# Kernel optimization log

Measured on AMD Instinct MI355X. Metric: run time of the kernel, lower is better.

## Reference

```python
import jax, jax.numpy as jnp
import numpy as np

V = 100000   # nodes
E = 1600000  # edges (avg degree 16)
LN = 64      # feat_dim
S = 8        # stat_dim
T = 4        # recurrence steps
MU = 0.9
N_EDGE_TYPES = 10


def _uniform_linear(kw, kb, fan_out, fan_in):
    # torch nn.Linear default init: U(-1/sqrt(fan_in), 1/sqrt(fan_in))
    lim = 1.0 / np.sqrt(fan_in)
    W = jax.random.uniform(kw, (fan_out, fan_in), jnp.float32, -lim, lim)
    b = jax.random.uniform(kb, (fan_out,), jnp.float32, -lim, lim)
    return W, b


def setup_inputs() -> dict:
    key = jax.random.key(0)
    ks = jax.random.split(key, 12)
    feat_Matrix = jax.random.normal(ks[0], (V, LN), jnp.float32)
    X_Node = jax.random.randint(ks[1], (E,), 1, V + 1, dtype=jnp.int64)   # 1-indexed
    X_Neis = jax.random.randint(ks[2], (E,), 1, V + 1, dtype=jnp.int64)   # 1-indexed
    edge_type_index = jax.random.randint(ks[3], (E,), 1, N_EDGE_TYPES + 1, dtype=jnp.int32)
    dg_list = jax.random.randint(ks[4], (E,), 1, 65).astype(jnp.float32)  # degrees >= 1
    H_init = jax.random.uniform(ks[5], (V, S), jnp.float32)  # torch.rand init of state
    W_xi, b_xi = _uniform_linear(ks[6], ks[7], S * S, 2 * LN + N_EDGE_TYPES)
    W_rou, b_rou = _uniform_linear(ks[8], ks[9], S, LN)
    W1, b1 = _uniform_linear(ks[10], ks[11], 1, S)
    return {
        "feat_Matrix": feat_Matrix, "X_Node": X_Node, "X_Neis": X_Neis,
        "edge_type_index": edge_type_index, "dg_list": dg_list, "H_init": H_init,
        "W_xi": W_xi, "b_xi": b_xi, "W_rou": W_rou, "b_rou": b_rou,
        "W1": W1, "b1": b1,
    }


def reference(feat_Matrix, X_Node, X_Neis, edge_type_index, dg_list, H_init,
              W_xi, b_xi, W_rou, b_rou, W1, b1):
    src = X_Node - 1           # 0-indexed source nodes
    dst = X_Neis - 1           # 0-indexed neighbor nodes (for embedding gather)
    node_emb = feat_Matrix[src]            # [E, LN]
    neis_emb = feat_Matrix[dst]            # [E, LN]
    et = jax.nn.one_hot(edge_type_index - 1, N_EDGE_TYPES, dtype=jnp.float32)
    X = jnp.concatenate([node_emb, neis_emb, et], axis=1)  # [E, 2*LN+10]

    # Xi(X): per-edge transition matrices A, constant across steps -> precompute
    A = jnp.tanh(X @ W_xi.T + b_xi).reshape(-1, S, S)
    A = A * (MU / S) / dg_list[:, None, None]              # [E, S, S]
    # Rou(neis_emb): per-edge bias b, constant across steps
    bias = jnp.tanh(neis_emb @ W_rou.T + b_rou)            # [E, S]

    def step(H, _):
        He = H[src]                                        # gather [E, S]
        out = jnp.einsum('eij,ej->ei', A, He) + bias       # per-edge small matmul
        # AggrSum: dense one-hot mask vs RAW 1-indexed X_Neis against range(0,V-1)
        # -> scatter by 1-indexed ids; ids == V fall out of range and are dropped.
        Hn = jax.ops.segment_sum(out, X_Neis, num_segments=V)
        return Hn, None

    H, _ = jax.lax.scan(step, H_init, None, length=T)      # [V, S]

    logits = (H @ W1.T + b1).squeeze(-1)                   # [V]
    attn = jax.nn.softmax(logits)                          # softmax over nodes
    graph_out = jnp.tanh(jnp.sum(H * attn[:, None], axis=0))  # [S]
    return graph_out
```

## Files before the change

kernel.cpp:

```cpp
#include <hip/hip_runtime.h>
#include <hip/hip_bf16.h>

constexpr int V   = 100000;
constexpr int E   = 1600000;
constexpr int NET = 10;
constexpr int KXW = 138;
constexpr int NB  = (V + 255) / 256;
constexpr int GN  = 8;
constexpr int NEB = E / 256;
constexpr float MUS   = 0.1125f;
constexpr float SP    = 0.025f;
constexpr float LOG2E = 1.44269504f;
constexpr float S2L   = 2.0f * SP * LOG2E;
constexpr float K7    = MUS / 7.0f;

typedef __attribute__((ext_vector_type(8))) short short8;
typedef __attribute__((ext_vector_type(4))) float float4v;

__device__ __forceinline__ float fast_tanh(float x) {
    return 1.0f - 2.0f * __builtin_amdgcn_rcpf(__expf(2.0f * x) + 1.0f);
}
__device__ __forceinline__ float bflo(unsigned u) { return __uint_as_float(u << 16); }
__device__ __forceinline__ float bfhi(unsigned u) { return __uint_as_float(u & 0xffff0000u); }
__device__ __forceinline__ short f2bf(float x) {
    union { __hip_bfloat16 b; short s; } u; u.b = __float2bfloat16(x); return u.s;
}

__device__ __forceinline__ float ub0(unsigned u) {
#if __has_builtin(__builtin_amdgcn_cvt_f32_ubyte0)
    return __builtin_amdgcn_cvt_f32_ubyte0(u);
#else
    return (float)(u & 0xff);
#endif
}
__device__ __forceinline__ float ub1(unsigned u) {
#if __has_builtin(__builtin_amdgcn_cvt_f32_ubyte1)
    return __builtin_amdgcn_cvt_f32_ubyte1(u);
#else
    return (float)((u >> 8) & 0xff);
#endif
}
__device__ __forceinline__ float ub2(unsigned u) {
#if __has_builtin(__builtin_amdgcn_cvt_f32_ubyte2)
    return __builtin_amdgcn_cvt_f32_ubyte2(u);
#else
    return (float)((u >> 16) & 0xff);
#endif
}
__device__ __forceinline__ float ub3(unsigned u) {
#if __has_builtin(__builtin_amdgcn_cvt_f32_ubyte3)
    return __builtin_amdgcn_cvt_f32_ubyte3(u);
#else
    return (float)(u >> 24);
#endif
}

__device__ __forceinline__ int dot8i4(unsigned a, unsigned b, int c) {
#if __has_builtin(__builtin_amdgcn_sdot8)
    return __builtin_amdgcn_sdot8((int)a, (int)b, c, false);
#else
    int r = c;
    #pragma unroll
    for (int j = 0; j < 8; ++j) {
        int av = ((int)(a << (28 - 4 * j))) >> 28;
        int bv = ((int)(b << (28 - 4 * j))) >> 28;
        r += av * bv;
    }
    return r;
#endif
}

__global__ __launch_bounds__(256) void histg_kernel(
    const int* __restrict__ xneis, int* __restrict__ countg,
    int* __restrict__ rank0)
{
    int e = blockIdx.x * 256 + threadIdx.x;
    if (e >= E) return;
    int g = blockIdx.x & (GN - 1);
    int nr = xneis[e];
    if (nr < V) rank0[e] = atomicAdd(&countg[g * V + nr], 1);
}

__global__ __launch_bounds__(256) void scanV_kernel(
    const int* __restrict__ countg, int* __restrict__ offg,
    int* __restrict__ cnt_tot, int* __restrict__ scanned, int* __restrict__ bsum)
{
    __shared__ int s[256];
    int tid = threadIdx.x;
    int i = blockIdx.x * 256 + tid;
    int c = 0;
    if (i < V) {
        int run = 0;
        #pragma unroll
        for (int g = 0; g < GN; ++g) {
            offg[g * V + i] = run;
            run += countg[g * V + i];
        }
        cnt_tot[i] = run;
        c = run;
    }
    s[tid] = c; __syncthreads();
    #pragma unroll
    for (int off = 1; off < 256; off <<= 1) {
        int t = (tid >= off) ? s[tid - off] : 0;
        __syncthreads();
        s[tid] += t;
        __syncthreads();
    }
    if (i < V) scanned[i] = s[tid] - c;
    if (tid == 255) bsum[blockIdx.x] = s[255];
}

__global__ __launch_bounds__(512) void scan_tops_kernel(
    const int* __restrict__ blocksum, int* __restrict__ tops, int* __restrict__ rowptr)
{
    __shared__ int s[512];
    int tid = threadIdx.x;
    int v = (tid < NB) ? blocksum[tid] : 0;
    s[tid] = v; __syncthreads();
    #pragma unroll
    for (int off = 1; off < 512; off <<= 1) {
        int t = (tid >= off) ? s[tid - off] : 0;
        __syncthreads();
        s[tid] += t;
        __syncthreads();
    }
    if (tid < NB) tops[tid] = s[tid] - v;
    if (tid == 511) rowptr[V] = s[511];
}

__global__ __launch_bounds__(256) void add_offsets_kernel(
    const int* __restrict__ scanned, const int* __restrict__ tops, int* __restrict__ rowptr)
{
    int i = blockIdx.x * 256 + threadIdx.x;
    if (i < V) rowptr[i] = scanned[i] + tops[blockIdx.x];
}

__global__ __launch_bounds__(256) void scatterA_kernel(
    const int* __restrict__ xnode, const int* __restrict__ xneis,
    const int* __restrict__ etype, const float* __restrict__ dg,
    const int* __restrict__ rowptr, const int* __restrict__ offg,
    const int* __restrict__ rank0, uint2* __restrict__ buc,
    int* __restrict__ bcnt)
{
    __shared__ int wcnt[4][8];
    __shared__ int woff[4][8];
    int tid = threadIdx.x;
    int lane = tid & 63, wv = tid >> 6;
    int e = blockIdx.x * 256 + tid;
    int g = blockIdx.x & (GN - 1);

    int nr = xneis[e];
    bool keep = (nr < V);
    int p = -1, r = 0;
    if (keep) {
        p = rowptr[nr] + offg[g * V + nr] + rank0[e];
        r = p >> 18;
    }

    unsigned rnk = 0;
    #pragma unroll
    for (int r8 = 0; r8 < 8; ++r8) {
        unsigned long long m = __ballot(keep && (r == r8));
        if (keep && r == r8)
            rnk = (unsigned)__popcll(m & ((1ull << lane) - 1ull));
        if (lane == 0) wcnt[wv][r8] = (int)__popcll(m);
    }
    __syncthreads();
    if (tid < 8) {
        int run = 0;
        #pragma unroll
        for (int w = 0; w < 4; ++w) { woff[w][tid] = run; run += wcnt[w][tid]; }
        bcnt[blockIdx.x * 8 + tid] = run;
    }
    __syncthreads();

    if (keep) {
        unsigned src = (unsigned)(xnode[e] - 1);
        unsigned et  = (unsigned)(etype[e] - 1);
        unsigned dgi = (unsigned)dg[e] - 1;
        unsigned meta = src | (et << 17) | (dgi << 21);
        int slot = blockIdx.x * 2048 + r * 256 + woff[wv][r] + (int)rnk;
        buc[slot] = make_uint2((unsigned)p, meta);
    }
}

__global__ __launch_bounds__(256) void drain_kernel(
    const uint2* __restrict__ buc, const int* __restrict__ bcnt,
    unsigned* __restrict__ pmeta)
{
    int r = blockIdx.x & 7;
    int nstride = (int)(gridDim.x >> 3);
    for (int sb = (int)(blockIdx.x >> 3); sb < NEB; sb += nstride) {
        int c = bcnt[sb * 8 + r];
        const uint2* seg = buc + (size_t)sb * 2048 + r * 256;
        for (int i = threadIdx.x; i < c; i += 256) {
            uint2 t = seg[i];
            pmeta[t.x] = t.y;
        }
    }
}

__global__ __launch_bounds__(256) void bsum_kernel(
    const float* __restrict__ feat, const int* __restrict__ count,
    const float* __restrict__ Wrou, const float* __restrict__ brou,
    const float* __restrict__ Hinit, float* __restrict__ Bsum,
    uint2* __restrict__ Hq0)
{
    __shared__ float Wl[512];
    __shared__ float bl[8];
    int tid = threadIdx.x;
    for (int i = tid; i < 512; i += 256) Wl[i] = Wrou[i];
    if (tid < 8) bl[tid] = brou[tid];
    __syncthreads();

    int v = blockIdx.x * 256 + tid;
    if (v >= V) return;
    int c = count[v];
    float out[8] = {0, 0, 0, 0, 0, 0, 0, 0};
    if (c > 0) {
        const float4* f4 = (const float4*)(feat + (size_t)(v - 1) * 64);
        float acc[8];
        #pragma unroll
        for (int s = 0; s < 8; ++s) acc[s] = bl[s];
        #pragma unroll 4
        for (int k = 0; k < 16; ++k) {
            float4 x = f4[k];
            #pragma unroll
            for (int s = 0; s < 8; ++s) {
                const float* w = &Wl[s * 64 + k * 4];
                acc[s] += x.x * w[0] + x.y * w[1] + x.z * w[2] + x.w * w[3];
            }
        }
        float fc = (float)c;
        #pragma unroll
        for (int s = 0; s < 8; ++s) out[s] = fc * fast_tanh(acc[s]);
    }
    float4* O = (float4*)(Bsum + (size_t)v * 8);
    O[0] = make_float4(out[0], out[1], out[2], out[3]);
    O[1] = make_float4(out[4], out[5], out[6], out[7]);

    const float4* Hh4 = (const float4*)(Hinit + (size_t)v * 8);
    float4 h0 = Hh4[0], h1 = Hh4[1];
    float hv[8] = {h0.x, h0.y, h0.z, h0.w, h1.x, h1.y, h1.z, h1.w};
    float mx = 0.0f;
    #pragma unroll
    for (int i = 0; i < 8; ++i) mx = fmaxf(mx, fabsf(hv[i]));
    float si = (mx > 0.0f) ? 7.0f / mx : 0.0f;
    unsigned w = 0;
    #pragma unroll
    for (int i = 0; i < 8; ++i)
        w |= ((unsigned)((int)rintf(hv[i] * si)) & 0xFu) << (4 * i);
    Hq0[v] = make_uint2(w, __float_as_uint(mx * (1.0f / 7.0f)));
}

__global__ __launch_bounds__(256) void pq_kernel(
    const float* __restrict__ feat, const float* __restrict__ Wxi,
    unsigned char* __restrict__ P8, ushort* __restrict__ Qb)
{
    const int lane = threadIdx.x & 63, wave = threadIdx.x >> 6;
    const int quad = lane >> 4, l16 = lane & 15;

    short8 bP[4][2], bQ[4][2];
    #pragma unroll
    for (int nt = 0; nt < 4; ++nt) {
        #pragma unroll
        for (int ks = 0; ks < 2; ++ks) {
            const float* wp = Wxi + (size_t)(nt * 16 + l16) * KXW + ks * 32 + quad * 8;
            short8 p, q;
            #pragma unroll
            for (int j = 0; j < 8; ++j) { p[j] = f2bf(wp[j]); q[j] = f2bf(wp[64 + j]); }
            bP[nt][ks] = p; bQ[nt][ks] = q;
        }
    }

    int t = blockIdx.x * 4 + wave;
    if (t >= V / 16) return;
    int v0 = t * 16;

    const float* fp = feat + (size_t)(v0 + l16) * 64 + quad * 8;
    short8 a0, a1;
    #pragma unroll
    for (int j = 0; j < 8; ++j) { a0[j] = f2bf(fp[j]); a1[j] = f2bf(fp[32 + j]); }

    float4v accP[4], accQ[4];
    #pragma unroll
    for (int nt = 0; nt < 4; ++nt) {
        float4v z = {0.f, 0.f, 0.f, 0.f};
        z = __builtin_amdgcn_mfma_f32_16x16x32_bf16(a0, bP[nt][0], z, 0, 0, 0);
        z = __builtin_amdgcn_mfma_f32_16x16x32_bf16(a1, bP[nt][1], z, 0, 0, 0);
        accP[nt] = z;
        float4v w = {0.f, 0.f, 0.f, 0.f};
        w = __builtin_amdgcn_mfma_f32_16x16x32_bf16(a0, bQ[nt][0], w, 0, 0, 0);
        w = __builtin_amdgcn_mfma_f32_16x16x32_bf16(a1, bQ[nt][1], w, 0, 0, 0);
        accQ[nt] = w;
    }

    #pragma unroll
    for (int r = 0; r < 4; ++r) {
        int row = v0 + quad * 4 + r;
        #pragma unroll
        for (int nt = 0; nt < 4; ++nt) {
            int col = nt * 16 + l16;
            int q8 = (int)rintf(accP[nt][r] * (1.0f / SP)) + 128;
            q8 = min(max(q8, 0), 255);
            P8[row * 64 + col] = (unsigned char)q8;
            Qb[row * 64 + col] = (ushort)f2bf(accQ[nt][r]);
        }
    }
}

__global__ __launch_bounds__(256) void amat_kernel(
    const unsigned* __restrict__ pmeta, const int* __restrict__ rowptr,
    const unsigned char* __restrict__ P8, const ushort* __restrict__ Qb,
    const float* __restrict__ Wxi, const float* __restrict__ bxi,
    const uint2* __restrict__ Hq0, const float* __restrict__ Bsum,
    unsigned* __restrict__ A4, uint2* __restrict__ HqOut)
{
    __shared__ float Wet2[NET * 64];
    int tid = threadIdx.x;
    for (int i = tid; i < NET * 64; i += 256) {
        int et = i >> 6, n = i & 63;
        Wet2[i] = 2.0f * LOG2E * (Wxi[n * KXW + 128 + et] + bxi[n]);
    }
    __syncthreads();

    int v = blockIdx.x * 4 + (tid >> 6);
    if (v >= V) return;
    int lane = tid & 63;
    int el = lane >> 3, s = lane & 7;

    const int off = rowptr[v];
    const int deg = rowptr[v + 1] - off;

    float q0, q1, q2, q3, q4, q5, q6, q7;
    {
        uint4 qu = *(const uint4*)(Qb + v * 64 + s * 8);
        const float B = 128.0f * SP, C = 2.0f * LOG2E;
        q0 = C * (bflo(qu.x) - B); q1 = C * (bfhi(qu.x) - B);
        q2 = C * (bflo(qu.y) - B); q3 = C * (bfhi(qu.y) - B);
        q4 = C * (bflo(qu.z) - B); q5 = C * (bfhi(qu.z) - B);
        q6 = C * (bflo(qu.w) - B); q7 = C * (bfhi(qu.w) - B);
    }

    float accD = 0.0f;

    for (int base = 0; base < deg; base += 64) {
        unsigned m_mine = 0;
        {
            int i1 = base + lane;
            if (i1 < deg) m_mine = pmeta[off + i1];
        }
        int nb = deg - base;
        for (int k = 0; k * 8 + el < nb && k < 8; ++k) {
            int ib = k * 8 + el;
            int i = base + ib;
            unsigned m = __shfl(m_mine, ib);
            int src = (int)(m & 0x1FFFF);
            int et  = (int)((m >> 17) & 0xF);

            uint2 pu = *(const uint2*)(P8 + src * 64 + s * 8);
            const float4* w4 = (const float4*)(&Wet2[et * 64 + s * 8]);
            float4 wa = w4[0], wb = w4[1];
            uint2 hq = Hq0[src];

            float r0 = __builtin_amdgcn_rcpf(__builtin_amdgcn_exp2f(fmaf(ub0(pu.x), S2L, q0 + wa.x)) + 1.0f);
            float r1 = __builtin_amdgcn_rcpf(__builtin_amdgcn_exp2f(fmaf(ub1(pu.x), S2L, q1 + wa.y)) + 1.0f);
            float r2 = __builtin_amdgcn_rcpf(__builtin_amdgcn_exp2f(fmaf(ub2(pu.x), S2L, q2 + wa.z)) + 1.0f);
            float r3 = __builtin_amdgcn_rcpf(__builtin_amdgcn_exp2f(fmaf(ub3(pu.x), S2L, q3 + wa.w)) + 1.0f);
            float r4 = __builtin_amdgcn_rcpf(__builtin_amdgcn_exp2f(fmaf(ub0(pu.y), S2L, q4 + wb.x)) + 1.0f);
            float r5 = __builtin_amdgcn_rcpf(__builtin_amdgcn_exp2f(fmaf(ub1(pu.y), S2L, q5 + wb.y)) + 1.0f);
            float r6 = __builtin_amdgcn_rcpf(__builtin_amdgcn_exp2f(fmaf(ub2(pu.y), S2L, q6 + wb.z)) + 1.0f);
            float r7 = __builtin_amdgcn_rcpf(__builtin_amdgcn_exp2f(fmaf(ub3(pu.y), S2L, q7 + wb.w)) + 1.0f);

            int n0 = (int)rintf(fmaf(r0, -14.0f, 7.0f));
            int n1 = (int)rintf(fmaf(r1, -14.0f, 7.0f));
            int n2 = (int)rintf(fmaf(r2, -14.0f, 7.0f));
            int n3 = (int)rintf(fmaf(r3, -14.0f, 7.0f));
            int n4 = (int)rintf(fmaf(r4, -14.0f, 7.0f));
            int n5 = (int)rintf(fmaf(r5, -14.0f, 7.0f));
            int n6 = (int)rintf(fmaf(r6, -14.0f, 7.0f));
            int n7 = (int)rintf(fmaf(r7, -14.0f, 7.0f));

            unsigned w = ((unsigned)n0 & 0xFu)        | (((unsigned)n1 & 0xFu) << 4)
                       | (((unsigned)n2 & 0xFu) << 8)  | (((unsigned)n3 & 0xFu) << 12)
                       | (((unsigned)n4 & 0xFu) << 16) | (((unsigned)n5 & 0xFu) << 20)
                       | (((unsigned)n6 & 0xFu) << 24) | (((unsigned)n7 & 0xFu) << 28);
            A4[(unsigned)(off + i) * 8u + (unsigned)s] = w;

            int dd = dot8i4(w, hq.x, 0);
            float rdg = __builtin_amdgcn_rcpf((float)((int)(m >> 21) + 1));
            accD = fmaf((float)dd, __uint_as_float(hq.y) * rdg, accD);
        }
    }
    accD += __shfl_xor(accD, 8);  accD += __shfl_xor(accD, 16); accD += __shfl_xor(accD, 32);
    float h1v = accD * K7 + Bsum[v * 8 + s];

    float mx = fabsf(h1v);
    mx = fmaxf(mx, __shfl_xor(mx, 1));
    mx = fmaxf(mx, __shfl_xor(mx, 2));
    mx = fmaxf(mx, __shfl_xor(mx, 4));
    float si = (mx > 0.0f) ? 7.0f / mx : 0.0f;
    unsigned nib = (unsigned)((int)rintf(h1v * si)) & 0xFu;
    unsigned b1 = __shfl(nib, lane + 1), b2 = __shfl(nib, lane + 2), b3 = __shfl(nib, lane + 3);
    unsigned b4 = __shfl(nib, lane + 4), b5 = __shfl(nib, lane + 5);
    unsigned b6 = __shfl(nib, lane + 6), b7 = __shfl(nib, lane + 7);
    if (lane == 0) {
        unsigned w = nib | (b1 << 4) | (b2 << 8) | (b3 << 12)
                   | (b4 << 16) | (b5 << 20) | (b6 << 24) | (b7 << 28);
        HqOut[v] = make_uint2(w, __float_as_uint(mx * (1.0f / 7.0f)));
    }
}

__global__ __launch_bounds__(256) void step_kernel(
    const uint2* __restrict__ HqIn, uint2* __restrict__ HqOut,
    const unsigned* __restrict__ pmeta, const int* __restrict__ rowptr,
    const unsigned* __restrict__ A4, const float* __restrict__ Bsum,
    const float* __restrict__ W1, const float* __restrict__ b1,
    float* __restrict__ logitsOut, float* __restrict__ HfpOut)
{
    int v = blockIdx.x * 64 + (threadIdx.x >> 2);
    if (v >= V) return;
    int q = threadIdx.x & 3;

    int p0 = rowptr[v], p1 = rowptr[v + 1];

    float accE0 = 0.0f, accO0 = 0.0f, accE1 = 0.0f, accO1 = 0.0f;
    int p = p0;
    for (; p + 1 < p1; p += 2) {
        unsigned m0 = pmeta[p], m1 = pmeta[p + 1];
        uint2 au0 = *(const uint2*)(A4 + (unsigned)p * 8u + (unsigned)(q * 2));
        uint2 au1 = *(const uint2*)(A4 + (unsigned)(p + 1) * 8u + (unsigned)(q * 2));
        uint2 hq0 = HqIn[m0 & 0x1FFFFu];
        uint2 hq1 = HqIn[m1 & 0x1FFFFu];

        int dE0 = dot8i4(au0.x, hq0.x, 0);
        int dO0 = dot8i4(au0.y, hq0.x, 0);
        float rdg0 = __builtin_amdgcn_rcpf((float)((int)(m0 >> 21) + 1));
        float sc0 = __uint_as_float(hq0.y) * rdg0;
        accE0 = fmaf((float)dE0, sc0, accE0);
        accO0 = fmaf((float)dO0, sc0, accO0);

        int dE1 = dot8i4(au1.x, hq1.x, 0);
        int dO1 = dot8i4(au1.y, hq1.x, 0);
        float rdg1 = __builtin_amdgcn_rcpf((float)((int)(m1 >> 21) + 1));
        float sc1 = __uint_as_float(hq1.y) * rdg1;
        accE1 = fmaf((float)dE1, sc1, accE1);
        accO1 = fmaf((float)dO1, sc1, accO1);
    }
    if (p < p1) {
        unsigned m = pmeta[p];
        uint2 au = *(const uint2*)(A4 + (unsigned)p * 8u + (unsigned)(q * 2));
        uint2 hq = HqIn[m & 0x1FFFFu];
        int dE = dot8i4(au.x, hq.x, 0);
        int dO = dot8i4(au.y, hq.x, 0);
        float rdg = __builtin_amdgcn_rcpf((float)((int)(m >> 21) + 1));
        float sc = __uint_as_float(hq.y) * rdg;
        accE0 = fmaf((float)dE, sc, accE0);
        accO0 = fmaf((float)dO, sc, accO0);
    }
    float accE = accE0 + accE1;
    float accO = accO0 + accO1;

    float hE = accE * K7 + Bsum[v * 8 + q * 2];
    float hO = accO * K7 + Bsum[v * 8 + q * 2 + 1];

    float mx = fmaxf(fabsf(hE), fabsf(hO));
    mx = fmaxf(mx, __shfl_xor(mx, 1));
    mx = fmaxf(mx, __shfl_xor(mx, 2));
    float si = (mx > 0.0f) ? 7.0f / mx : 0.0f;
    unsigned nE = (unsigned)((int)rintf(hE * si)) & 0xFu;
    unsigned nO = (unsigned)((int)rintf(hO * si)) & 0xFu;
    unsigned wq = (nE | (nO << 4)) << (8 * q);
    wq |= __shfl_xor(wq, 1);
    wq |= __shfl_xor(wq, 2);
    if (q == 0)
        HqOut[v] = make_uint2(wq, __float_as_uint(mx * (1.0f / 7.0f)));
    if (HfpOut != nullptr)
        *(float2*)(HfpOut + v * 8 + q * 2) = make_float2(hE, hO);
    if (logitsOut != nullptr) {
        float t = hE * W1[q * 2] + hO * W1[q * 2 + 1];
        t += __shfl_xor(t, 1); t += __shfl_xor(t, 2);
        if (q == 0) logitsOut[v] = t + b1[0];
    }
}

__global__ __launch_bounds__(256) void sum_kernel(
    const float* __restrict__ H, const float* __restrict__ logits,
    float* __restrict__ partial)
{
    float m = -INFINITY, se = 0.0f;
    float sh[8] = {0, 0, 0, 0, 0, 0, 0, 0};
    for (int v = blockIdx.x * 256 + threadIdx.x; v < V; v += 64 * 256) {
        float l = logits[v];
        float mn = fmaxf(m, l);
        float a = __expf(m - mn);
        float w = __expf(l - mn);
        se = se * a + w;
        const float4* H4 = (const float4*)(H + (size_t)v * 8);
        float4 h0 = H4[0], h1 = H4[1];
        sh[0] = sh[0] * a + w * h0.x; sh[1] = sh[1] * a + w * h0.y;
        sh[2] = sh[2] * a + w * h0.z; sh[3] = sh[3] * a + w * h0.w;
        sh[4] = sh[4] * a + w * h1.x; sh[5] = sh[5] * a + w * h1.y;
        sh[6] = sh[6] * a + w * h1.z; sh[7] = sh[7] * a + w * h1.w;
        m = mn;
    }
    #pragma unroll
    for (int o = 1; o < 64; o <<= 1) {
        float mo = __shfl_xor(m, o), seo = __shfl_xor(se, o);
        float sho[8];
        #pragma unroll
        for (int i = 0; i < 8; ++i) sho[i] = __shfl_xor(sh[i], o);
        float mn = fmaxf(m, mo);
        float a = __expf(m - mn), b = __expf(mo - mn);
        se = se * a + seo * b;
        #pragma unroll
        for (int i = 0; i < 8; ++i) sh[i] = sh[i] * a + sho[i] * b;
        m = mn;
    }
    __shared__ float sm[4][10];
    int wv = threadIdx.x >> 6;
    if ((threadIdx.x & 63) == 0) {
        sm[wv][0] = m; sm[wv][9] = se;
        #pragma unroll
        for (int i = 0; i < 8; ++i) sm[wv][1 + i] = sh[i];
    }
    __syncthreads();
    if (threadIdx.x == 0) {
        float M = sm[0][0], SE = 0.0f, SH[8] = {0, 0, 0, 0, 0, 0, 0, 0};
        #pragma unroll
        for (int w2 = 1; w2 < 4; ++w2) M = fmaxf(M, sm[w2][0]);
        #pragma unroll
        for (int w2 = 0; w2 < 4; ++w2) {
            float a = __expf(sm[w2][0] - M);
            SE += sm[w2][9] * a;
            #pragma unroll
            for (int i = 0; i < 8; ++i) SH[i] += sm[w2][1 + i] * a;
        }
        partial[blockIdx.x * 12 + 0] = M;
        partial[blockIdx.x * 12 + 9] = SE;
        #pragma unroll
        for (int i = 0; i < 8; ++i) partial[blockIdx.x * 12 + 1 + i] = SH[i];
    }
}

__global__ void final_kernel(const float* __restrict__ partial, float* __restrict__ out)
{
    int lane = threadIdx.x;
    float m = partial[lane * 12 + 0];
    float se = partial[lane * 12 + 9];
    float sh[8];
    #pragma unroll
    for (int i = 0; i < 8; ++i) sh[i] = partial[lane * 12 + 1 + i];
    #pragma unroll
    for (int o = 1; o < 64; o <<= 1) {
        float mo = __shfl_xor(m, o), seo = __shfl_xor(se, o);
        float sho[8];
        #pragma unroll
        for (int i = 0; i < 8; ++i) sho[i] = __shfl_xor(sh[i], o);
        float mn = fmaxf(m, mo);
        float a = __expf(m - mn), b = __expf(mo - mn);
        se = se * a + seo * b;
        #pragma unroll
        for (int i = 0; i < 8; ++i) sh[i] = sh[i] * a + sho[i] * b;
        m = mn;
    }
    if (lane < 8) out[lane] = tanhf(sh[lane] / se);
}

extern "C" void kernel_launch(void* const* d_in, const int* in_sizes, int n_in,
                              void* d_out, int out_size, void* d_ws, size_t ws_size,
                              hipStream_t stream)
{
    const float* feat  = (const float*)d_in[0];
    const int*   xnode = (const int*)d_in[1];
    const int*   xneis = (const int*)d_in[2];
    const int*   etype = (const int*)d_in[3];
    const float* dg    = (const float*)d_in[4];
    const float* Hinit = (const float*)d_in[5];
    const float* Wxi   = (const float*)d_in[6];
    const float* bxi   = (const float*)d_in[7];
    const float* Wrou  = (const float*)d_in[8];
    const float* brou  = (const float*)d_in[9];
    const float* W1    = (const float*)d_in[10];
    const float* b1    = (const float*)d_in[11];

    char* ws = (char*)d_ws;
    auto alloc = [&](size_t bytes) -> char* {
        char* p = ws; ws += (bytes + 255) & ~(size_t)255; return p;
    };
    unsigned* A4      = (unsigned*)alloc((size_t)E * 32);
    uint2*    buc     = (uint2*)alloc((size_t)NEB * 2048 * 8);
    unsigned char* P8 = (unsigned char*)alloc((size_t)V * 64);
    ushort*   Qb      = (ushort*)alloc((size_t)V * 64 * 2);
    unsigned* pmeta   = (unsigned*)alloc((size_t)E * 4);
    int*      rank0   = (int*)alloc((size_t)E * 4);
    int*      countg  = (int*)alloc((size_t)GN * V * 4);
    int*      offg    = (int*)alloc((size_t)GN * V * 4);
    int*      bcnt    = (int*)alloc((size_t)NEB * 8 * 4);
    int*      cnt     = (int*)alloc((size_t)V * 4);
    int*      scanned = (int*)alloc((size_t)V * 4);
    int*      rowptr  = (int*)alloc((size_t)(V + 1) * 4);
    int*      bsumT   = (int*)alloc(512 * 4);
    int*      topsT   = (int*)alloc(512 * 4);
    uint2*    Hq0     = (uint2*)alloc((size_t)V * 8);
    uint2*    HqA     = (uint2*)alloc((size_t)V * 8);
    uint2*    HqB     = (uint2*)alloc((size_t)V * 8);
    float*    Hfp     = (float*)alloc((size_t)V * 8 * 4);
    float*    Bsum    = (float*)alloc((size_t)V * 8 * 4);
    float*    logits  = (float*)alloc((size_t)V * 4);
    float*    spart   = (float*)alloc(64 * 12 * 4);

    hipMemsetAsync(countg, 0, (size_t)GN * V * 4, stream);
    histg_kernel<<<NEB, 256, 0, stream>>>(xneis, countg, rank0);
    scanV_kernel<<<NB, 256, 0, stream>>>(countg, offg, cnt, scanned, bsumT);
    scan_tops_kernel<<<1, 512, 0, stream>>>(bsumT, topsT, rowptr);
    add_offsets_kernel<<<NB, 256, 0, stream>>>(scanned, topsT, rowptr);
    scatterA_kernel<<<NEB, 256, 0, stream>>>(xnode, xneis, etype, dg,
                                             rowptr, offg, rank0, buc, bcnt);
    drain_kernel<<<2048, 256, 0, stream>>>(buc, bcnt, pmeta);
    pq_kernel<<<(V / 16 + 3) / 4, 256, 0, stream>>>(feat, Wxi, P8, Qb);
    bsum_kernel<<<NB, 256, 0, stream>>>(feat, cnt, Wrou, brou, Hinit,
                                        Bsum, Hq0);
    amat_kernel<<<(V + 3) / 4, 256, 0, stream>>>(pmeta, rowptr, P8, Qb, Wxi, bxi,
                                                 Hq0, Bsum, A4, HqA);

    const uint2* Hcur = HqA;
    uint2* bufs[2] = {HqB, HqA};
    for (int t = 0; t < 3; ++t) {
        uint2* Hn = bufs[t & 1];
        float* lg  = (t == 2) ? logits : nullptr;
        float* hf  = (t == 2) ? Hfp : nullptr;
        step_kernel<<<(V + 63) / 64, 256, 0, stream>>>(Hcur, Hn, pmeta, rowptr,
                                                       A4, Bsum, W1, b1, lg, hf);
        Hcur = Hn;
    }

    sum_kernel<<<64, 256, 0, stream>>>(Hfp, logits, spart);
    final_kernel<<<1, 64, 0, stream>>>(spart, (float*)d_out);
}
```

Measured before the change: 404.7 us.

## Merge histogram with PQ projection, fuse scan with bias sum, unroll step loop

The histogram kernel and the P/Q feature projection kernel now share one grid, with block-index ranges picking the role, so the independent work runs concurrently. The per-node count scan is fused with the Rou bias-sum and H_init quantization kernel, which drops the separate count buffer and a launch. The step kernel's edge loop is unrolled by four with four accumulator pairs to expose more memory-level parallelism, and the bias is read as a float2. The changes cut launch count and idle gaps between small kernels, at the cost of higher register pressure in the step kernel and a heterogeneous mixed-role grid.

```diff
diff --git a/kernel.cpp b/kernel.cpp
--- a/kernel.cpp
+++ b/kernel.cpp
@@ -8,6 +8,7 @@
 constexpr int NB  = (V + 255) / 256;
 constexpr int GN  = 8;
 constexpr int NEB = E / 256;
+constexpr int NPQ = (V / 16 + 3) / 4;
 constexpr float MUS   = 0.1125f;
 constexpr float SP    = 0.025f;
 constexpr float LOG2E = 1.44269504f;
@@ -70,194 +71,20 @@
 #endif
 }
 
-__global__ __launch_bounds__(256) void histg_kernel(
+__global__ __launch_bounds__(256) void histg_pq_kernel(
     const int* __restrict__ xneis, int* __restrict__ countg,
-    int* __restrict__ rank0)
-{
-    int e = blockIdx.x * 256 + threadIdx.x;
-    if (e >= E) return;
-    int g = blockIdx.x & (GN - 1);
-    int nr = xneis[e];
-    if (nr < V) rank0[e] = atomicAdd(&countg[g * V + nr], 1);
-}
-
-__global__ __launch_bounds__(256) void scanV_kernel(
-    const int* __restrict__ countg, int* __restrict__ offg,
-    int* __restrict__ cnt_tot, int* __restrict__ scanned, int* __restrict__ bsum)
-{
-    __shared__ int s[256];
-    int tid = threadIdx.x;
-    int i = blockIdx.x * 256 + tid;
-    int c = 0;
-    if (i < V) {
-        int run = 0;
-        #pragma unroll
-        for (int g = 0; g < GN; ++g) {
-            offg[g * V + i] = run;
-            run += countg[g * V + i];
-        }
-        cnt_tot[i] = run;
-        c = run;
-    }
-    s[tid] = c; __syncthreads();
-    #pragma unroll
-    for (int off = 1; off < 256; off <<= 1) {
-        int t = (tid >= off) ? s[tid - off] : 0;
-        __syncthreads();
-        s[tid] += t;
-        __syncthreads();
-    }
-    if (i < V) scanned[i] = s[tid] - c;
-    if (tid == 255) bsum[blockIdx.x] = s[255];
-}
-
-__global__ __launch_bounds__(512) void scan_tops_kernel(
-    const int* __restrict__ blocksum, int* __restrict__ tops, int* __restrict__ rowptr)
-{
-    __shared__ int s[512];
-    int tid = threadIdx.x;
-    int v = (tid < NB) ? blocksum[tid] : 0;
-    s[tid] = v; __syncthreads();
-    #pragma unroll
-    for (int off = 1; off < 512; off <<= 1) {
-        int t = (tid >= off) ? s[tid - off] : 0;
-        __syncthreads();
-        s[tid] += t;
-        __syncthreads();
-    }
-    if (tid < NB) tops[tid] = s[tid] - v;
-    if (tid == 511) rowptr[V] = s[511];
-}
-
-__global__ __launch_bounds__(256) void add_offsets_kernel(
-    const int* __restrict__ scanned, const int* __restrict__ tops, int* __restrict__ rowptr)
-{
-    int i = blockIdx.x * 256 + threadIdx.x;
-    if (i < V) rowptr[i] = scanned[i] + tops[blockIdx.x];
-}
-
-__global__ __launch_bounds__(256) void scatterA_kernel(
-    const int* __restrict__ xnode, const int* __restrict__ xneis,
-    const int* __restrict__ etype, const float* __restrict__ dg,
-    const int* __restrict__ rowptr, const int* __restrict__ offg,
-    const int* __restrict__ rank0, uint2* __restrict__ buc,
-    int* __restrict__ bcnt)
-{
-    __shared__ int wcnt[4][8];
-    __shared__ int woff[4][8];
-    int tid = threadIdx.x;
-    int lane = tid & 63, wv = tid >> 6;
-    int e = blockIdx.x * 256 + tid;
-    int g = blockIdx.x & (GN - 1);
-
-    int nr = xneis[e];
-    bool keep = (nr < V);
-    int p = -1, r = 0;
-    if (keep) {
-        p = rowptr[nr] + offg[g * V + nr] + rank0[e];
-        r = p >> 18;
-    }
-
-    unsigned rnk = 0;
-    #pragma unroll
-    for (int r8 = 0; r8 < 8; ++r8) {
-        unsigned long long m = __ballot(keep && (r == r8));
-        if (keep && r == r8)
-            rnk = (unsigned)__popcll(m & ((1ull << lane) - 1ull));
-        if (lane == 0) wcnt[wv][r8] = (int)__popcll(m);
-    }
-    __syncthreads();
-    if (tid < 8) {
-        int run = 0;
-        #pragma unroll
-        for (int w = 0; w < 4; ++w) { woff[w][tid] = run; run += wcnt[w][tid]; }
-        bcnt[blockIdx.x * 8 + tid] = run;
-    }
-    __syncthreads();
-
-    if (keep) {
-        unsigned src = (unsigned)(xnode[e] - 1);
-        unsigned et  = (unsigned)(etype[e] - 1);
-        unsigned dgi = (unsigned)dg[e] - 1;
-        unsigned meta = src | (et << 17) | (dgi << 21);
-        int slot = blockIdx.x * 2048 + r * 256 + woff[wv][r] + (int)rnk;
-        buc[slot] = make_uint2((unsigned)p, meta);
-    }
-}
-
-__global__ __launch_bounds__(256) void drain_kernel(
-    const uint2* __restrict__ buc, const int* __restrict__ bcnt,
-    unsigned* __restrict__ pmeta)
-{
-    int r = blockIdx.x & 7;
-    int nstride = (int)(gridDim.x >> 3);
-    for (int sb = (int)(blockIdx.x >> 3); sb < NEB; sb += nstride) {
-        int c = bcnt[sb * 8 + r];
-        const uint2* seg = buc + (size_t)sb * 2048 + r * 256;
-        for (int i = threadIdx.x; i < c; i += 256) {
-            uint2 t = seg[i];
-            pmeta[t.x] = t.y;
-        }
-    }
-}
-
-__global__ __launch_bounds__(256) void bsum_kernel(
-    const float* __restrict__ feat, const int* __restrict__ count,
-    const float* __restrict__ Wrou, const float* __restrict__ brou,
-    const float* __restrict__ Hinit, float* __restrict__ Bsum,
-    uint2* __restrict__ Hq0)
-{
-    __shared__ float Wl[512];
-    __shared__ float bl[8];
-    int tid = threadIdx.x;
-    for (int i = tid; i < 512; i += 256) Wl[i] = Wrou[i];
-    if (tid < 8) bl[tid] = brou[tid];
-    __syncthreads();
-
-    int v = blockIdx.x * 256 + tid;
-    if (v >= V) return;
-    int c = count[v];
-    float out[8] = {0, 0, 0, 0, 0, 0, 0, 0};
-    if (c > 0) {
-        const float4* f4 = (const float4*)(feat + (size_t)(v - 1) * 64);
-        float acc[8];
-        #pragma unroll
-        for (int s = 0; s < 8; ++s) acc[s] = bl[s];
-        #pragma unroll 4
-        for (int k = 0; k < 16; ++k) {
-            float4 x = f4[k];
-            #pragma unroll
-            for (int s = 0; s < 8; ++s) {
-                const float* w = &Wl[s * 64 + k * 4];
-                acc[s] += x.x * w[0] + x.y * w[1] + x.z * w[2] + x.w * w[3];
-            }
-        }
-        float fc = (float)c;
-        #pragma unroll
-        for (int s = 0; s < 8; ++s) out[s] = fc * fast_tanh(acc[s]);
-    }
-    float4* O = (float4*)(Bsum + (size_t)v * 8);
-    O[0] = make_float4(out[0], out[1], out[2], out[3]);
-    O[1] = make_float4(out[4], out[5], out[6], out[7]);
-
-    const float4* Hh4 = (const float4*)(Hinit + (size_t)v * 8);
-    float4 h0 = Hh4[0], h1 = Hh4[1];
-    float hv[8] = {h0.x, h0.y, h0.z, h0.w, h1.x, h1.y, h1.z, h1.w};
-    float mx = 0.0f;
-    #pragma unroll
-    for (int i = 0; i < 8; ++i) mx = fmaxf(mx, fabsf(hv[i]));
-    float si = (mx > 0.0f) ? 7.0f / mx : 0.0f;
-    unsigned w = 0;
-    #pragma unroll
-    for (int i = 0; i < 8; ++i)
-        w |= ((unsigned)((int)rintf(hv[i] * si)) & 0xFu) << (4 * i);
-    Hq0[v] = make_uint2(w, __float_as_uint(mx * (1.0f / 7.0f)));
-}
-
-__global__ __launch_bounds__(256) void pq_kernel(
+    int* __restrict__ rank0,
     const float* __restrict__ feat, const float* __restrict__ Wxi,
     unsigned char* __restrict__ P8, ushort* __restrict__ Qb)
 {
+    if (blockIdx.x < NEB) {
+        int e = blockIdx.x * 256 + threadIdx.x;
+        int g = blockIdx.x & (GN - 1);
+        int nr = xneis[e];
+        if (nr < V) rank0[e] = atomicAdd(&countg[g * V + nr], 1);
+        return;
+    }
+    int bid = blockIdx.x - NEB;
     const int lane = threadIdx.x & 63, wave = threadIdx.x >> 6;
     const int quad = lane >> 4, l16 = lane & 15;
 
@@ -274,7 +101,7 @@
         }
     }
 
-    int t = blockIdx.x * 4 + wave;
+    int t = bid * 4 + wave;
     if (t >= V / 16) return;
     int v0 = t * 16;
 
@@ -306,6 +133,170 @@
             q8 = min(max(q8, 0), 255);
             P8[row * 64 + col] = (unsigned char)q8;
             Qb[row * 64 + col] = (ushort)f2bf(accQ[nt][r]);
+        }
+    }
+}
+
+__global__ __launch_bounds__(256) void scanV_bsum_kernel(
+    const int* __restrict__ countg, int* __restrict__ offg,
+    int* __restrict__ scanned, int* __restrict__ bsumT,
+    const float* __restrict__ feat, const float* __restrict__ Wrou,
+    const float* __restrict__ brou, const float* __restrict__ Hinit,
+    float* __restrict__ Bsum, uint2* __restrict__ Hq0)
+{
+    __shared__ int s[256];
+    __shared__ float Wl[512];
+    __shared__ float bl[8];
+    int tid = threadIdx.x;
+    for (int i = tid; i < 512; i += 256) Wl[i] = Wrou[i];
+    if (tid < 8) bl[tid] = brou[tid];
+
+    int v = blockIdx.x * 256 + tid;
+    int c = 0;
+    if (v < V) {
+        int run = 0;
+        #pragma unroll
+        for (int g = 0; g < GN; ++g) {
+            offg[g * V + v] = run;
+            run += countg[g * V + v];
+        }
+        c = run;
+    }
+    s[tid] = c; __syncthreads();
+    #pragma unroll
+    for (int off = 1; off < 256; off <<= 1) {
+        int t = (tid >= off) ? s[tid - off] : 0;
+        __syncthreads();
+        s[tid] += t;
+        __syncthreads();
+    }
+    if (v < V) scanned[v] = s[tid] - c;
+    if (tid == 255) bsumT[blockIdx.x] = s[255];
+
+    if (v >= V) return;
+    float out[8] = {0, 0, 0, 0, 0, 0, 0, 0};
+    if (c > 0) {
+        const float4* f4 = (const float4*)(feat + (size_t)(v - 1) * 64);
+        float acc[8];
+        #pragma unroll
+        for (int ss = 0; ss < 8; ++ss) acc[ss] = bl[ss];
+        #pragma unroll 4
+        for (int k = 0; k < 16; ++k) {
+            float4 x = f4[k];
+            #pragma unroll
+            for (int ss = 0; ss < 8; ++ss) {
+                const float* w = &Wl[ss * 64 + k * 4];
+                acc[ss] += x.x * w[0] + x.y * w[1] + x.z * w[2] + x.w * w[3];
+            }
+        }
+        float fc = (float)c;
+        #pragma unroll
+        for (int ss = 0; ss < 8; ++ss) out[ss] = fc * fast_tanh(acc[ss]);
+    }
+    float4* O = (float4*)(Bsum + (size_t)v * 8);
+    O[0] = make_float4(out[0], out[1], out[2], out[3]);
+    O[1] = make_float4(out[4], out[5], out[6], out[7]);
+
+    const float4* Hh4 = (const float4*)(Hinit + (size_t)v * 8);
+    float4 h0 = Hh4[0], h1 = Hh4[1];
+    float hv[8] = {h0.x, h0.y, h0.z, h0.w, h1.x, h1.y, h1.z, h1.w};
+    float mx = 0.0f;
+    #pragma unroll
+    for (int i = 0; i < 8; ++i) mx = fmaxf(mx, fabsf(hv[i]));
+    float si = (mx > 0.0f) ? 7.0f / mx : 0.0f;
+    unsigned w = 0;
+    #pragma unroll
+    for (int i = 0; i < 8; ++i)
+        w |= ((unsigned)((int)rintf(hv[i] * si)) & 0xFu) << (4 * i);
+    Hq0[v] = make_uint2(w, __float_as_uint(mx * (1.0f / 7.0f)));
+}
+
+__global__ __launch_bounds__(512) void scan_tops_kernel(
+    const int* __restrict__ blocksum, int* __restrict__ tops, int* __restrict__ rowptr)
+{
+    __shared__ int s[512];
+    int tid = threadIdx.x;
+    int v = (tid < NB) ? blocksum[tid] : 0;
+    s[tid] = v; __syncthreads();
+    #pragma unroll
+    for (int off = 1; off < 512; off <<= 1) {
+        int t = (tid >= off) ? s[tid - off] : 0;
+        __syncthreads();
+        s[tid] += t;
+        __syncthreads();
+    }
+    if (tid < NB) tops[tid] = s[tid] - v;
+    if (tid == 511) rowptr[V] = s[511];
+}
+
+__global__ __launch_bounds__(256) void add_offsets_kernel(
+    const int* __restrict__ scanned, const int* __restrict__ tops, int* __restrict__ rowptr)
+{
+    int i = blockIdx.x * 256 + threadIdx.x;
+    if (i < V) rowptr[i] = scanned[i] + tops[blockIdx.x];
+}
+
+__global__ __launch_bounds__(256) void scatterA_kernel(
+    const int* __restrict__ xnode, const int* __restrict__ xneis,
+    const int* __restrict__ etype, const float* __restrict__ dg,
+    const int* __restrict__ rowptr, const int* __restrict__ offg,
+    const int* __restrict__ rank0, uint2* __restrict__ buc,
+    int* __restrict__ bcnt)
+{
+    __shared__ int wcnt[4][8];
+    __shared__ int woff[4][8];
+    int tid = threadIdx.x;
+    int lane = tid & 63, wv = tid >> 6;
+    int e = blockIdx.x * 256 + tid;
+    int g = blockIdx.x & (GN - 1);
+
+    int nr = xneis[e];
+    bool keep = (nr < V);
+    int p = -1, r = 0;
+    if (keep) {
+        p = rowptr[nr] + offg[g * V + nr] + rank0[e];
+        r = p >> 18;
+    }
+
+    unsigned rnk = 0;
+    #pragma unroll
+    for (int r8 = 0; r8 < 8; ++r8) {
+        unsigned long long m = __ballot(keep && (r == r8));
+        if (keep && r == r8)
+            rnk = (unsigned)__popcll(m & ((1ull << lane) - 1ull));
+        if (lane == 0) wcnt[wv][r8] = (int)__popcll(m);
+    }
+    __syncthreads();
+    if (tid < 8) {
+        int run = 0;
+        #pragma unroll
+        for (int w = 0; w < 4; ++w) { woff[w][tid] = run; run += wcnt[w][tid]; }
+        bcnt[blockIdx.x * 8 + tid] = run;
+    }
+    __syncthreads();
+
+    if (keep) {
+        unsigned src = (unsigned)(xnode[e] - 1);
+        unsigned et  = (unsigned)(etype[e] - 1);
+        unsigned dgi = (unsigned)dg[e] - 1;
+        unsigned meta = src | (et << 17) | (dgi << 21);
+        int slot = blockIdx.x * 2048 + r * 256 + woff[wv][r] + (int)rnk;
+        buc[slot] = make_uint2((unsigned)p, meta);
+    }
+}
+
+__global__ __launch_bounds__(256) void drain_kernel(
+    const uint2* __restrict__ buc, const int* __restrict__ bcnt,
+    unsigned* __restrict__ pmeta)
+{
+    int r = blockIdx.x & 7;
+    int nstride = (int)(gridDim.x >> 3);
+    for (int sb = (int)(blockIdx.x >> 3); sb < NEB; sb += nstride) {
+        int c = bcnt[sb * 8 + r];
+        const uint2* seg = buc + (size_t)sb * 2048 + r * 256;
+        for (int i = threadIdx.x; i < c; i += 256) {
+            uint2 t = seg[i];
+            pmeta[t.x] = t.y;
         }
     }
 }
@@ -425,45 +416,61 @@
 
     int p0 = rowptr[v], p1 = rowptr[v + 1];
 
-    float accE0 = 0.0f, accO0 = 0.0f, accE1 = 0.0f, accO1 = 0.0f;
+    float aE0 = 0.f, aO0 = 0.f, aE1 = 0.f, aO1 = 0.f;
+    float aE2 = 0.f, aO2 = 0.f, aE3 = 0.f, aO3 = 0.f;
     int p = p0;
+    for (; p + 3 < p1; p += 4) {
+        unsigned m0 = pmeta[p],     m1 = pmeta[p + 1];
+        unsigned m2 = pmeta[p + 2], m3 = pmeta[p + 3];
+        uint2 au0 = *(const uint2*)(A4 + (unsigned)p * 8u + (unsigned)(q * 2));
+        uint2 au1 = *(const uint2*)(A4 + (unsigned)(p + 1) * 8u + (unsigned)(q * 2));
+        uint2 au2 = *(const uint2*)(A4 + (unsigned)(p + 2) * 8u + (unsigned)(q * 2));
+        uint2 au3 = *(const uint2*)(A4 + (unsigned)(p + 3) * 8u + (unsigned)(q * 2));
+        uint2 hq0 = HqIn[m0 & 0x1FFFFu];
+        uint2 hq1 = HqIn[m1 & 0x1FFFFu];
+        uint2 hq2 = HqIn[m2 & 0x1FFFFu];
+        uint2 hq3 = HqIn[m3 & 0x1FFFFu];
+
+        float sc0 = __uint_as_float(hq0.y) * __builtin_amdgcn_rcpf((float)((int)(m0 >> 21) + 1));
+        aE0 = fmaf((float)dot8i4(au0.x, hq0.x, 0), sc0, aE0);
+        aO0 = fmaf((float)dot8i4(au0.y, hq0.x, 0), sc0, aO0);
+        float sc1 = __uint_as_float(hq1.y) * __builtin_amdgcn_rcpf((float)((int)(m1 >> 21) + 1));
+        aE1 = fmaf((float)dot8i4(au1.x, hq1.x, 0), sc1, aE1);
+        aO1 = fmaf((float)dot8i4(au1.y, hq1.x, 0), sc1, aO1);
+        float sc2 = __uint_as_float(hq2.y) * __builtin_amdgcn_rcpf((float)((int)(m2 >> 21) + 1));
+        aE2 = fmaf((float)dot8i4(au2.x, hq2.x, 0), sc2, aE2);
+        aO2 = fmaf((float)dot8i4(au2.y, hq2.x, 0), sc2, aO2);
+        float sc3 = __uint_as_float(hq3.y) * __builtin_amdgcn_rcpf((float)((int)(m3 >> 21) + 1));
+        aE3 = fmaf((float)dot8i4(au3.x, hq3.x, 0), sc3, aE3);
+        aO3 = fmaf((float)dot8i4(au3.y, hq3.x, 0), sc3, aO3);
+    }
     for (; p + 1 < p1; p += 2) {
         unsigned m0 = pmeta[p], m1 = pmeta[p + 1];
         uint2 au0 = *(const uint2*)(A4 + (unsigned)p * 8u + (unsigned)(q * 2));
         uint2 au1 = *(const uint2*)(A4 + (unsigned)(p + 1) * 8u + (unsigned)(q * 2));
         uint2 hq0 = HqIn[m0 & 0x1FFFFu];
         uint2 hq1 = HqIn[m1 & 0x1FFFFu];
-
-        int dE0 = dot8i4(au0.x, hq0.x, 0);
-        int dO0 = dot8i4(au0.y, hq0.x, 0);
-        float rdg0 = __builtin_amdgcn_rcpf((float)((int)(m0 >> 21) + 1));
-        float sc0 = __uint_as_float(hq0.y) * rdg0;
-        accE0 = fmaf((float)dE0, sc0, accE0);
-        accO0 = fmaf((float)dO0, sc0, accO0);
-
-        int dE1 = dot8i4(au1.x, hq1.x, 0);
-        int dO1 = dot8i4(au1.y, hq1.x, 0);
-        float rdg1 = __builtin_amdgcn_rcpf((float)((int)(m1 >> 21) + 1));
-        float sc1 = __uint_as_float(hq1.y) * rdg1;
-        accE1 = fmaf((float)dE1, sc1, accE1);
-        accO1 = fmaf((float)dO1, sc1, accO1);
+        float sc0 = __uint_as_float(hq0.y) * __builtin_amdgcn_rcpf((float)((int)(m0 >> 21) + 1));
+        aE0 = fmaf((float)dot8i4(au0.x, hq0.x, 0), sc0, aE0);
+        aO0 = fmaf((float)dot8i4(au0.y, hq0.x, 0), sc0, aO0);
+        float sc1 = __uint_as_float(hq1.y) * __builtin_amdgcn_rcpf((float)((int)(m1 >> 21) + 1));
+        aE1 = fmaf((float)dot8i4(au1.x, hq1.x, 0), sc1, aE1);
+        aO1 = fmaf((float)dot8i4(au1.y, hq1.x, 0), sc1, aO1);
     }
     if (p < p1) {
         unsigned m = pmeta[p];
         uint2 au = *(const uint2*)(A4 + (unsigned)p * 8u + (unsigned)(q * 2));
         uint2 hq = HqIn[m & 0x1FFFFu];
-        int dE = dot8i4(au.x, hq.x, 0);
-        int dO = dot8i4(au.y, hq.x, 0);
-        float rdg = __builtin_amdgcn_rcpf((float)((int)(m >> 21) + 1));
-        float sc = __uint_as_float(hq.y) * rdg;
-        accE0 = fmaf((float)dE, sc, accE0);
-        accO0 = fmaf((float)dO, sc, accO0);
-    }
-    float accE = accE0 + accE1;
-    float accO = accO0 + accO1;
-
-    float hE = accE * K7 + Bsum[v * 8 + q * 2];
-    float hO = accO * K7 + Bsum[v * 8 + q * 2 + 1];
+        float sc = __uint_as_float(hq.y) * __builtin_amdgcn_rcpf((float)((int)(m >> 21) + 1));
+        aE0 = fmaf((float)dot8i4(au.x, hq.x, 0), sc, aE0);
+        aO0 = fmaf((float)dot8i4(au.y, hq.x, 0), sc, aO0);
+    }
+    float accE = (aE0 + aE1) + (aE2 + aE3);
+    float accO = (aO0 + aO1) + (aO2 + aO3);
+
+    float2 bs = *(const float2*)(Bsum + v * 8 + q * 2);
+    float hE = accE * K7 + bs.x;
+    float hO = accO * K7 + bs.y;
 
     float mx = fmaxf(fabsf(hE), fabsf(hO));
     mx = fmaxf(mx, __shfl_xor(mx, 1));
@@ -598,7 +605,6 @@
     int*      countg  = (int*)alloc((size_t)GN * V * 4);
     int*      offg    = (int*)alloc((size_t)GN * V * 4);
     int*      bcnt    = (int*)alloc((size_t)NEB * 8 * 4);
-    int*      cnt     = (int*)alloc((size_t)V * 4);
     int*      scanned = (int*)alloc((size_t)V * 4);
     int*      rowptr  = (int*)alloc((size_t)(V + 1) * 4);
     int*      bsumT   = (int*)alloc(512 * 4);
@@ -612,16 +618,16 @@
     float*    spart   = (float*)alloc(64 * 12 * 4);
 
     hipMemsetAsync(countg, 0, (size_t)GN * V * 4, stream);
-    histg_kernel<<<NEB, 256, 0, stream>>>(xneis, countg, rank0);
-    scanV_kernel<<<NB, 256, 0, stream>>>(countg, offg, cnt, scanned, bsumT);
+    histg_pq_kernel<<<NEB + NPQ, 256, 0, stream>>>(xneis, countg, rank0,
+                                                   feat, Wxi, P8, Qb);
+    scanV_bsum_kernel<<<NB, 256, 0, stream>>>(countg, offg, scanned, bsumT,
+                                              feat, Wrou, brou, Hinit,
+                                              Bsum, Hq0);
     scan_tops_kernel<<<1, 512, 0, stream>>>(bsumT, topsT, rowptr);
     add_offsets_kernel<<<NB, 256, 0, stream>>>(scanned, topsT, rowptr);
     scatterA_kernel<<<NEB, 256, 0, stream>>>(xnode, xneis, etype, dg,
                                              rowptr, offg, rank0, buc, bcnt);
     drain_kernel<<<2048, 256, 0, stream>>>(buc, bcnt, pmeta);
-    pq_kernel<<<(V / 16 + 3) / 4, 256, 0, stream>>>(feat, Wxi, P8, Qb);
-    bsum_kernel<<<NB, 256, 0, stream>>>(feat, cnt, Wrou, brou, Hinit,
-                                        Bsum, Hq0);
     amat_kernel<<<(V + 3) / 4, 256, 0, stream>>>(pmeta, rowptr, P8, Qb, Wxi, bxi,
                                                  Hq0, Bsum, A4, HqA);
 
```

Result: faster. 394.9 us (-2.4%).
